# Optimization experiments

Hardware: AMD Instinct MI355X
Metric: run time of the kernel (lower is better)

Reference implementation:

```python
import jax, jax.numpy as jnp
import numpy as np

NUM_CLASSES = 1000
MARGIN = 1.0
COS_EPS = 1e-8   # torch F.cosine_similarity eps
NORM_EPS = 1e-12 # torch F.normalize eps


def setup_inputs() -> dict:
    key = jax.random.key(0)
    k1, k2 = jax.random.split(key)
    N, D = 65536, 256
    embeddings = jax.random.normal(k1, (N, D), dtype=jnp.float32)
    labels = jax.random.randint(k2, (N,), 0, NUM_CLASSES)
    return {"embeddings": embeddings, "labels": labels}


def reference(embeddings, labels):
    N = embeddings.shape[0]
    # L2-normalize embeddings (torch F.normalize with eps clamp on norm)
    e_norm = jnp.maximum(jnp.linalg.norm(embeddings, axis=1, keepdims=True), NORM_EPS)
    e = embeddings / e_norm  # [N, D], unit rows

    # Per-class mean of normalized embeddings; zero vector for empty classes
    sums = jax.ops.segment_sum(e, labels, num_segments=NUM_CLASSES)          # [C, D]
    counts = jax.ops.segment_sum(jnp.ones((N,), e.dtype), labels,
                                 num_segments=NUM_CLASSES)                    # [C]
    centers = sums / jnp.maximum(counts, 1.0)[:, None]                        # [C, D]

    # cosine_similarity(e_i, center_j) = (e_i . c_j) / max(||e_i||*||c_j||, eps)
    # ||e_i|| == 1 (up to the normalize clamp), so denom = max(||c_j||, eps)
    c_norm = jnp.linalg.norm(centers, axis=1)                                 # [C]
    denom = jnp.maximum(c_norm, COS_EPS)
    sims = (e @ centers.T) / denom[None, :]                                   # [N, C]

    rows = jnp.arange(N)
    pos = jnp.square(sims[rows, labels] - 1.0)                                # [N]
    neg_all = jnp.square(jax.nn.relu(MARGIN - sims))                          # [N, C]
    neg_at_label = neg_all[rows, labels]                                      # [N]
    neg = (neg_all.sum(axis=1) - neg_at_label) / (NUM_CLASSES - 1)            # [N]

    return jnp.mean(pos + neg)
```

## Files before the change

kernel.cpp:

```cpp
#include <hip/hip_runtime.h>
#include <hip/hip_bf16.h>

#define NROWS 65536
#define DIM   256
#define NCLS  1000
#define CPAD  1024

typedef __attribute__((ext_vector_type(8))) short bf16x8;
typedef __attribute__((ext_vector_type(4))) float f32x4;

__device__ inline unsigned short f2bf(float x) {
    unsigned int u = __builtin_bit_cast(unsigned int, x);
    unsigned int lsb = (u >> 16) & 1u;
    u += 0x7fffu + lsb;
    return (unsigned short)(u >> 16);
}

__device__ inline float bf2f(unsigned short u) {
    unsigned int v = ((unsigned int)u) << 16;
    return __builtin_bit_cast(float, v);
}

__device__ inline void gload_lds16(const void* g, void* l) {
    __builtin_amdgcn_global_load_lds(
        (const __attribute__((address_space(1))) unsigned int*)g,
        (__attribute__((address_space(3))) unsigned int*)l, 16, 0, 0);
}

__global__ __launch_bounds__(256) void k_norm_acc(
    const float* __restrict__ emb, unsigned short* __restrict__ e,
    float* __restrict__ sums, unsigned int* __restrict__ counts,
    float* __restrict__ acc, unsigned int* __restrict__ done)
{
    const int tid = threadIdx.x;
    const int bid = blockIdx.x;
    if (tid < 128) sums[bid * 128 + tid] = 0.0f;
    if (bid < 16 && tid < 64) counts[bid * 64 + tid] = 0u;
    if (bid == 0 && tid == 0) { *acc = 0.0f; *done = 0u; }

    const int wave = tid >> 6, lane = tid & 63;
    const int w = bid * 4 + wave;

    #pragma unroll
    for (int i = 0; i < 2; ++i) {
        const int rbase = w * 8 + i * 4;
        float4 v[4];
        #pragma unroll
        for (int r = 0; r < 4; ++r)
            v[r] = ((const float4*)(emb + (size_t)(rbase + r) * DIM))[lane];
        float ss[4];
        #pragma unroll
        for (int r = 0; r < 4; ++r)
            ss[r] = v[r].x*v[r].x + v[r].y*v[r].y + v[r].z*v[r].z + v[r].w*v[r].w;
        #pragma unroll
        for (int off = 1; off < 64; off <<= 1) {
            #pragma unroll
            for (int r = 0; r < 4; ++r) ss[r] += __shfl_xor(ss[r], off);
        }
        #pragma unroll
        for (int r = 0; r < 4; ++r) {
            float inv = 1.0f / fmaxf(sqrtf(ss[r]), 1e-12f);
            ushort4 u;
            u.x = f2bf(v[r].x * inv); u.y = f2bf(v[r].y * inv);
            u.z = f2bf(v[r].z * inv); u.w = f2bf(v[r].w * inv);
            ((ushort4*)(e + (size_t)(rbase + r) * DIM))[lane] = u;
        }
    }
}

__global__ __launch_bounds__(256) void k_gather_partial(
    const unsigned short* __restrict__ e, const int* __restrict__ labels,
    float* __restrict__ sums, unsigned int* __restrict__ counts)
{
    const int c   = blockIdx.x >> 1;
    const int h   = blockIdx.x & 1;
    const int tid = threadIdx.x;
    const int wave = tid >> 6, lane = tid & 63;

    __shared__ float part[4][DIM];
    __shared__ unsigned int cnt_s[4];

    const int base = h * (NROWS / 2);
    float a0 = 0.f, a1 = 0.f, a2 = 0.f, a3 = 0.f;
    unsigned int cnt = 0;

    for (int it = 0; it < (NROWS / 2) / 256 / 8; ++it) {
        int lb[8];
        #pragma unroll
        for (int u = 0; u < 8; ++u)
            lb[u] = labels[base + (it * 8 + u) * 256 + wave * 64 + lane];
        #pragma unroll
        for (int u = 0; u < 8; ++u) {
            unsigned long long m = __ballot(lb[u] == c);
            cnt += (unsigned int)__popcll(m);
            int rb = base + (it * 8 + u) * 256 + wave * 64;
            while (m) {
                int b = __ffsll((long long)m) - 1;  m &= m - 1;
                ushort4 v = ((const ushort4*)(e + (size_t)(rb + b) * DIM))[lane];
                a0 += bf2f(v.x); a1 += bf2f(v.y); a2 += bf2f(v.z); a3 += bf2f(v.w);
            }
        }
    }
    ((float4*)part[wave])[lane] = make_float4(a0, a1, a2, a3);
    if (lane == 0) cnt_s[wave] = cnt;
    __syncthreads();

    float s = part[0][tid] + part[1][tid] + part[2][tid] + part[3][tid];
    atomicAdd(&sums[(size_t)c * DIM + tid], s);
    if (tid == 0)
        atomicAdd(&counts[c], cnt_s[0] + cnt_s[1] + cnt_s[2] + cnt_s[3]);
}

__global__ __launch_bounds__(256) void k_centers(
    const float* __restrict__ sums, const unsigned int* __restrict__ counts,
    unsigned short* __restrict__ cs)
{
    int gid  = blockIdx.x * 256 + threadIdx.x;
    int c    = gid >> 6;
    int lane = gid & 63;
    float4 v = ((const float4*)(sums + (size_t)c * DIM))[lane];
    float ic = 1.0f / fmaxf((float)counts[c], 1.0f);
    v.x *= ic; v.y *= ic; v.z *= ic; v.w *= ic;
    float ss = v.x*v.x + v.y*v.y + v.z*v.z + v.w*v.w;
    #pragma unroll
    for (int off = 1; off < 64; off <<= 1) ss += __shfl_xor(ss, off);
    float sc = 1.0f / fmaxf(sqrtf(ss), 1e-8f);
    ushort4 u;
    u.x = f2bf(v.x * sc); u.y = f2bf(v.y * sc);
    u.z = f2bf(v.z * sc); u.w = f2bf(v.w * sc);
    ((ushort4*)(cs + (size_t)c * DIM))[lane] = u;
}

#define TMB 128
#define TCB 128

__global__ __launch_bounds__(256, 2) void k_loss_mfma(
    const unsigned short* __restrict__ e, const unsigned short* __restrict__ cs,
    const int* __restrict__ labels, float* __restrict__ acc,
    unsigned int* __restrict__ done, float* __restrict__ out)
{
    __shared__ __align__(16) unsigned short a_s[2][TMB * 64];
    __shared__ __align__(16) unsigned short b_s[2][TCB * 64];
    __shared__ float red_s[4];

    const int tid  = threadIdx.x;
    const int row0 = blockIdx.x * TMB;
    const int wave = tid >> 6, lane = tid & 63;
    const int wm = wave >> 1, wn = wave & 1;
    const int l16 = lane & 15, q = lane >> 4;
    const int st_r = lane >> 3;
    const int st_s = (lane & 7) ^ st_r;

    int labv[16];
    #pragma unroll
    for (int mi = 0; mi < 4; ++mi)
        #pragma unroll
        for (int rg = 0; rg < 4; ++rg)
            labv[mi * 4 + rg] = labels[row0 + wm*64 + mi*16 + q*4 + rg];

    #pragma unroll
    for (int kc = 0; kc < 2; ++kc)
        #pragma unroll
        for (int ch = 0; ch < 4; ++ch) {
            int chunk = wave * 4 + ch;
            int row   = chunk * 8 + st_r;
            gload_lds16(&e[(size_t)(row0 + row) * DIM + kc * 64 + st_s * 8],
                        &a_s[kc][chunk * 512]);
        }
    bf16x8 af2[4][2], af3[4][2];
    #pragma unroll
    for (int mi = 0; mi < 4; ++mi) {
        const unsigned short* pa =
            e + (size_t)(row0 + wm*64 + mi*16 + l16) * DIM + 128 + q * 8;
        af2[mi][0] = *(const bf16x8*)pa;
        af2[mi][1] = *(const bf16x8*)(pa + 32);
        af3[mi][0] = *(const bf16x8*)(pa + 64);
        af3[mi][1] = *(const bf16x8*)(pa + 96);
    }
    #pragma unroll
    for (int ch = 0; ch < 4; ++ch) {
        int chunk = wave * 4 + ch;
        int row   = chunk * 8 + st_r;
        gload_lds16(&cs[(size_t)row * DIM + st_s * 8], &b_s[0][chunk * 512]);
    }
    __syncthreads();

    float la_bulk = 0.0f, la_corr = 0.0f;
    const float KN = 1.0f / 999.0f;

    for (int cb = 0; cb < CPAD / TCB; ++cb) {
        f32x4 accf[4][4];
        #pragma unroll
        for (int mi = 0; mi < 4; ++mi)
            #pragma unroll
            for (int ni = 0; ni < 4; ++ni)
                accf[mi][ni] = (f32x4){0.f, 0.f, 0.f, 0.f};

        #pragma unroll
        for (int kc = 0; kc < 4; ++kc) {
            if (cb < 7 || kc < 3) {
                const int cb2 = (kc == 3) ? cb + 1 : cb;
                const int kc2 = (kc + 1) & 3;
                #pragma unroll
                for (int ch = 0; ch < 4; ++ch) {
                    int chunk = wave * 4 + ch;
                    int row   = chunk * 8 + st_r;
                    gload_lds16(&cs[(size_t)(cb2 * TCB + row) * DIM + kc2 * 64 + st_s * 8],
                                &b_s[(kc + 1) & 1][chunk * 512]);
                }
            }
            const unsigned short* bs = b_s[kc & 1];
            #pragma unroll
            for (int kk = 0; kk < 2; ++kk) {
                bf16x8 af[4], bfr[4];
                #pragma unroll
                for (int mi = 0; mi < 4; ++mi) {
                    if (kc == 0 || kc == 1) {
                        int rowA = wm*64 + mi*16 + l16;
                        af[mi] = *(const bf16x8*)&a_s[kc][
                            rowA*64 + (((kk*4 + q) ^ (rowA & 7)) * 8)];
                    } else if (kc == 2) {
                        af[mi] = af2[mi][kk];
                    } else {
                        af[mi] = af3[mi][kk];
                    }
                }
                #pragma unroll
                for (int ni = 0; ni < 4; ++ni) {
                    int rowB = wn*64 + ni*16 + l16;
                    bfr[ni] = *(const bf16x8*)&bs[rowB*64 + (((kk*4 + q) ^ (rowB & 7)) * 8)];
                }
                #pragma unroll
                for (int mi = 0; mi < 4; ++mi)
                    #pragma unroll
                    for (int ni = 0; ni < 4; ++ni)
                        accf[mi][ni] = __builtin_amdgcn_mfma_f32_16x16x32_bf16(
                            af[mi], bfr[ni], accf[mi][ni], 0, 0, 0);
            }
            __syncthreads();
        }

        #pragma unroll
        for (int mi = 0; mi < 4; ++mi)
            #pragma unroll
            for (int rg = 0; rg < 4; ++rg) {
                #pragma unroll
                for (int ni = 0; ni < 4; ++ni) {
                    float t = 1.0f - accf[mi][ni][rg];
                    la_bulk += t * t;
                }
                int lr = labv[mi*4 + rg] - cb*128 - wn*64 - l16;
                if ((lr & ~48) == 0) {
                    int nih = lr >> 4;
                    float sv = (nih == 0) ? accf[mi][0][rg] :
                               (nih == 1) ? accf[mi][1][rg] :
                               (nih == 2) ? accf[mi][2][rg] : accf[mi][3][rg];
                    float t = 1.0f - sv;
                    la_corr += t * t;
                }
            }
    }

    float la = la_bulk * KN + la_corr * (1.0f - KN);
    #pragma unroll
    for (int off = 32; off >= 1; off >>= 1) la += __shfl_xor(la, off);
    if (lane == 0) red_s[wave] = la;
    __syncthreads();
    if (tid == 0) {
        atomicAdd(acc, red_s[0] + red_s[1] + red_s[2] + red_s[3]);
        __threadfence();
        unsigned int t = atomicAdd(done, 1u);
        if (t == (unsigned int)(NROWS / TMB) - 1u) {
            float v = atomicAdd(acc, 0.0f);
            out[0] = v * (1.0f / (float)NROWS) - 24.0f * (1.0f / 999.0f);
        }
    }
}

extern "C" void kernel_launch(void* const* d_in, const int* in_sizes, int n_in,
                              void* d_out, int out_size, void* d_ws, size_t ws_size,
                              hipStream_t stream)
{
    const float* emb    = (const float*)d_in[0];
    const int*   labels = (const int*)d_in[1];
    float*       out    = (float*)d_out;
    char*        ws     = (char*)d_ws;

    const size_t OFF_CS   = (size_t)NROWS * DIM * 2;
    const size_t OFF_SUMS = OFF_CS + (size_t)CPAD * DIM * 2;
    const size_t OFF_CNT  = OFF_SUMS + (size_t)CPAD * DIM * 4;
    const size_t OFF_ACC  = OFF_CNT + (size_t)CPAD * 4;
    const size_t OFF_DONE = OFF_ACC + 16;

    unsigned short* e      = (unsigned short*)ws;
    unsigned short* cs     = (unsigned short*)(ws + OFF_CS);
    float*          sums   = (float*)(ws + OFF_SUMS);
    unsigned int*   counts = (unsigned int*)(ws + OFF_CNT);
    float*          acc    = (float*)(ws + OFF_ACC);
    unsigned int*   done   = (unsigned int*)(ws + OFF_DONE);

    k_norm_acc      <<<NROWS / 32, 256, 0, stream>>>(emb, e, sums, counts, acc, done);
    k_gather_partial<<<NCLS * 2, 256, 0, stream>>>(e, labels, sums, counts);
    k_centers       <<<CPAD / 4, 256, 0, stream>>>(sums, counts, cs);
    k_loss_mfma     <<<NROWS / TMB, 256, 0, stream>>>(e, cs, labels, acc, done, out);
}
```

Before: 166.3 us.

## Keep full A rows in registers and deepen center-tile LDS pipeline to four stages

Each wave now owns 32 rows and computes them against all 128 centers of a tile, with the whole K=256 slice of its A rows held in registers, so the A tile no longer goes through LDS. The freed LDS holds a 4-stage ring of center chunks, prefetched three steps ahead. Each step syncs with an explicit vmcnt wait plus s_barrier instead of a trailing __syncthreads. In exchange, the extra A fragments and the 2x8 accumulator tile raise register pressure, and the loads past the last tile wrap to center row 0, which is wasted work.

```diff
diff --git a/kernel.cpp b/kernel.cpp
--- a/kernel.cpp
+++ b/kernel.cpp
@@ -139,122 +139,110 @@
     const int* __restrict__ labels, float* __restrict__ acc,
     unsigned int* __restrict__ done, float* __restrict__ out)
 {
-    __shared__ __align__(16) unsigned short a_s[2][TMB * 64];
-    __shared__ __align__(16) unsigned short b_s[2][TCB * 64];
+    __shared__ __align__(16) unsigned short b_s[4][TCB * 64];
     __shared__ float red_s[4];
 
     const int tid  = threadIdx.x;
     const int row0 = blockIdx.x * TMB;
     const int wave = tid >> 6, lane = tid & 63;
-    const int wm = wave >> 1, wn = wave & 1;
     const int l16 = lane & 15, q = lane >> 4;
     const int st_r = lane >> 3;
     const int st_s = (lane & 7) ^ st_r;
 
-    int labv[16];
-    #pragma unroll
-    for (int mi = 0; mi < 4; ++mi)
+    int labv[8];
+    #pragma unroll
+    for (int mi = 0; mi < 2; ++mi)
         #pragma unroll
         for (int rg = 0; rg < 4; ++rg)
-            labv[mi * 4 + rg] = labels[row0 + wm*64 + mi*16 + q*4 + rg];
-
-    #pragma unroll
-    for (int kc = 0; kc < 2; ++kc)
+            labv[mi * 4 + rg] = labels[row0 + wave*32 + mi*16 + q*4 + rg];
+
+    bf16x8 af[4][2][2];
+    #pragma unroll
+    for (int mi = 0; mi < 2; ++mi) {
+        const unsigned short* pa =
+            e + (size_t)(row0 + wave*32 + mi*16 + l16) * DIM + q * 8;
+        #pragma unroll
+        for (int kc = 0; kc < 4; ++kc)
+            #pragma unroll
+            for (int kk = 0; kk < 2; ++kk)
+                af[kc][mi][kk] = *(const bf16x8*)(pa + kc*64 + kk*32);
+    }
+
+    #pragma unroll
+    for (int pt = 0; pt < 3; ++pt)
         #pragma unroll
         for (int ch = 0; ch < 4; ++ch) {
             int chunk = wave * 4 + ch;
-            int row   = chunk * 8 + st_r;
-            gload_lds16(&e[(size_t)(row0 + row) * DIM + kc * 64 + st_s * 8],
-                        &a_s[kc][chunk * 512]);
-        }
-    bf16x8 af2[4][2], af3[4][2];
-    #pragma unroll
-    for (int mi = 0; mi < 4; ++mi) {
-        const unsigned short* pa =
-            e + (size_t)(row0 + wm*64 + mi*16 + l16) * DIM + 128 + q * 8;
-        af2[mi][0] = *(const bf16x8*)pa;
-        af2[mi][1] = *(const bf16x8*)(pa + 32);
-        af3[mi][0] = *(const bf16x8*)(pa + 64);
-        af3[mi][1] = *(const bf16x8*)(pa + 96);
-    }
-    #pragma unroll
-    for (int ch = 0; ch < 4; ++ch) {
-        int chunk = wave * 4 + ch;
-        int row   = chunk * 8 + st_r;
-        gload_lds16(&cs[(size_t)row * DIM + st_s * 8], &b_s[0][chunk * 512]);
-    }
+            gload_lds16(&cs[(size_t)(chunk*8 + st_r) * DIM + pt*64 + st_s*8],
+                        &b_s[pt][chunk * 512]);
+        }
     __syncthreads();
 
     float la_bulk = 0.0f, la_corr = 0.0f;
     const float KN = 1.0f / 999.0f;
 
     for (int cb = 0; cb < CPAD / TCB; ++cb) {
-        f32x4 accf[4][4];
-        #pragma unroll
-        for (int mi = 0; mi < 4; ++mi)
-            #pragma unroll
-            for (int ni = 0; ni < 4; ++ni)
+        f32x4 accf[2][8];
+        #pragma unroll
+        for (int mi = 0; mi < 2; ++mi)
+            #pragma unroll
+            for (int ni = 0; ni < 8; ++ni)
                 accf[mi][ni] = (f32x4){0.f, 0.f, 0.f, 0.f};
 
         #pragma unroll
         for (int kc = 0; kc < 4; ++kc) {
-            if (cb < 7 || kc < 3) {
-                const int cb2 = (kc == 3) ? cb + 1 : cb;
-                const int kc2 = (kc + 1) & 3;
+            __builtin_amdgcn_sched_barrier(0);
+            asm volatile("s_waitcnt vmcnt(8)" ::: "memory");
+            __builtin_amdgcn_s_barrier();
+            __builtin_amdgcn_sched_barrier(0);
+
+            {
+                const int t2  = cb * 4 + kc + 3;
+                const int cb2 = t2 >> 2, kc2 = t2 & 3;
                 #pragma unroll
                 for (int ch = 0; ch < 4; ++ch) {
                     int chunk = wave * 4 + ch;
-                    int row   = chunk * 8 + st_r;
-                    gload_lds16(&cs[(size_t)(cb2 * TCB + row) * DIM + kc2 * 64 + st_s * 8],
-                                &b_s[(kc + 1) & 1][chunk * 512]);
-                }
-            }
-            const unsigned short* bs = b_s[kc & 1];
+                    int crow  = (cb2 * TCB + chunk * 8 + st_r) & (CPAD - 1);
+                    gload_lds16(&cs[(size_t)crow * DIM + kc2*64 + st_s*8],
+                                &b_s[kc2][chunk * 512]);
+                }
+            }
+
             #pragma unroll
             for (int kk = 0; kk < 2; ++kk) {
-                bf16x8 af[4], bfr[4];
-                #pragma unroll
-                for (int mi = 0; mi < 4; ++mi) {
-                    if (kc == 0 || kc == 1) {
-                        int rowA = wm*64 + mi*16 + l16;
-                        af[mi] = *(const bf16x8*)&a_s[kc][
-                            rowA*64 + (((kk*4 + q) ^ (rowA & 7)) * 8)];
-                    } else if (kc == 2) {
-                        af[mi] = af2[mi][kk];
-                    } else {
-                        af[mi] = af3[mi][kk];
-                    }
-                }
-                #pragma unroll
-                for (int ni = 0; ni < 4; ++ni) {
-                    int rowB = wn*64 + ni*16 + l16;
-                    bfr[ni] = *(const bf16x8*)&bs[rowB*64 + (((kk*4 + q) ^ (rowB & 7)) * 8)];
-                }
-                #pragma unroll
-                for (int mi = 0; mi < 4; ++mi)
+                bf16x8 bfr[8];
+                #pragma unroll
+                for (int ni = 0; ni < 8; ++ni) {
+                    int rowB = ni * 16 + l16;
+                    bfr[ni] = *(const bf16x8*)&b_s[kc][
+                        rowB * 64 + (((kk*4 + q) ^ (rowB & 7)) * 8)];
+                }
+                #pragma unroll
+                for (int mi = 0; mi < 2; ++mi)
                     #pragma unroll
-                    for (int ni = 0; ni < 4; ++ni)
+                    for (int ni = 0; ni < 8; ++ni)
                         accf[mi][ni] = __builtin_amdgcn_mfma_f32_16x16x32_bf16(
-                            af[mi], bfr[ni], accf[mi][ni], 0, 0, 0);
-            }
-            __syncthreads();
-        }
-
-        #pragma unroll
-        for (int mi = 0; mi < 4; ++mi)
+                            af[kc][mi][kk], bfr[ni], accf[mi][ni], 0, 0, 0);
+            }
+        }
+
+        #pragma unroll
+        for (int mi = 0; mi < 2; ++mi)
             #pragma unroll
             for (int rg = 0; rg < 4; ++rg) {
                 #pragma unroll
-                for (int ni = 0; ni < 4; ++ni) {
+                for (int ni = 0; ni < 8; ++ni) {
                     float t = 1.0f - accf[mi][ni][rg];
                     la_bulk += t * t;
                 }
-                int lr = labv[mi*4 + rg] - cb*128 - wn*64 - l16;
-                if ((lr & ~48) == 0) {
+                int lr = labv[mi*4 + rg] - cb*TCB - l16;
+                if ((lr & ~112) == 0) {
                     int nih = lr >> 4;
-                    float sv = (nih == 0) ? accf[mi][0][rg] :
-                               (nih == 1) ? accf[mi][1][rg] :
-                               (nih == 2) ? accf[mi][2][rg] : accf[mi][3][rg];
+                    float sv = (nih & 4)
+                        ? ((nih & 2) ? ((nih & 1) ? accf[mi][7][rg] : accf[mi][6][rg])
+                                     : ((nih & 1) ? accf[mi][5][rg] : accf[mi][4][rg]))
+                        : ((nih & 2) ? ((nih & 1) ? accf[mi][3][rg] : accf[mi][2][rg])
+                                     : ((nih & 1) ? accf[mi][1][rg] : accf[mi][0][rg]));
                     float t = 1.0f - sv;
                     la_corr += t * t;
                 }
```

Measured after the change: 160.7 us. -3.3%, faster.
